# Optimization experiments

Measured on AMD Instinct MI355X. Metric: run time of the kernel, lower is better.

Reference implementation:

```python
import jax, jax.numpy as jnp
import numpy as np

DIM = 384
WIN = 64
HEADS = 12
B_ = 4096


def setup_inputs() -> dict:
    key = jax.random.key(0)
    k1, k2, k3, k4, k5 = jax.random.split(key, 5)
    x = jax.random.normal(k1, (B_, WIN, DIM), dtype=jnp.float32)
    # torch Linear weights: qkv.weight [3*dim, dim], proj.weight [dim, dim], proj.bias [dim]
    qkv_w = jax.random.normal(k2, (3 * DIM, DIM), dtype=jnp.float32) * (DIM ** -0.5)
    proj_w = jax.random.normal(k3, (DIM, DIM), dtype=jnp.float32) * (DIM ** -0.5)
    proj_b = jax.random.normal(k4, (DIM,), dtype=jnp.float32) * 0.02
    bias_table = jax.random.normal(k5, (2 * WIN - 1, HEADS), dtype=jnp.float32) * 0.02
    return {"x": x, "qkv_w": qkv_w, "proj_w": proj_w, "proj_b": proj_b,
            "bias_table": bias_table}


def reference(x, qkv_w, proj_w, proj_b, bias_table):
    B, N, C = x.shape
    H = HEADS
    hd = C // H
    scale = hd ** -0.5
    # qkv projection (torch: x @ W.T), split into q,k,v [B,H,N,hd]
    qkv = jnp.einsum('bnc,dc->bnd', x, qkv_w)
    qkv = qkv.reshape(B, N, 3, H, hd).transpose(2, 0, 3, 1, 4)
    q, k, v = qkv[0] * scale, qkv[1], qkv[2]
    attn = jnp.einsum('bhnd,bhmd->bhnm', q, k)  # [B,H,N,N]
    # relative position bias: index [N,N] into table [2W-1,H]
    coords = jnp.arange(N)
    rel_idx = coords[:, None] - coords[None, :] + (N - 1)  # [N,N]
    bias = bias_table[rel_idx]  # [N,N,H]
    attn = attn + bias.transpose(2, 0, 1)[None]
    attn = jax.nn.softmax(attn, axis=-1)
    out = jnp.einsum('bhnm,bhmd->bhnd', attn, v)
    out = out.transpose(0, 2, 1, 3).reshape(B, N, C)
    out = jnp.einsum('bnc,dc->bnd', out, proj_w) + proj_b
    return out
```

## Files before the change

### kernel.cpp

```cpp
#include <hip/hip_runtime.h>
#include <stdint.h>

#define DIM 384
#define WIN 64
#define HEADS 12
#define HD 32
#define NWIN 4096

typedef _Float16 f16;
typedef unsigned int u32;
typedef _Float16 half8 __attribute__((ext_vector_type(8)));
typedef _Float16 half4 __attribute__((ext_vector_type(4)));
typedef float floatx4 __attribute__((ext_vector_type(4)));

#define AS1 __attribute__((address_space(1)))
#define AS3 __attribute__((address_space(3)))

__device__ __forceinline__ void gl_lds16(const void* g, void* l) {
    __builtin_amdgcn_global_load_lds((const AS1 u32*)g, (AS3 u32*)l, 16, 0, 0);
}

__global__ void cvt_kernel(const float* __restrict__ in, f16* __restrict__ out, long n4) {
    long i = (long)blockIdx.x * blockDim.x + threadIdx.x;
    const long stride = (long)gridDim.x * blockDim.x;
    for (; i < n4; i += stride) {
        float4 v = ((const float4*)in)[i];
        half4 h;
        h[0] = (f16)v.x; h[1] = (f16)v.y; h[2] = (f16)v.z; h[3] = (f16)v.w;
        ((half4*)out)[i] = h;
    }
}

__global__ void pack_w_kernel(const float* __restrict__ w, f16* __restrict__ Bp) {
    const int t = blockIdx.x * 256 + threadIdx.x;
    const int colb = t / 9216;
    const int r1 = t % 9216;
    const int s = r1 / 768;
    const int r2 = r1 % 768;
    const int kc = r2 / 192, u = r2 % 192;
    const float* sp = w + (size_t)(colb * 192 + u) * DIM + s * 32 + kc * 8;
    float4 a = *(const float4*)sp;
    float4 b = *(const float4*)(sp + 4);
    half8 o;
    o[0] = (f16)a.x; o[1] = (f16)a.y; o[2] = (f16)a.z; o[3] = (f16)a.w;
    o[4] = (f16)b.x; o[5] = (f16)b.y; o[6] = (f16)b.z; o[7] = (f16)b.w;
    *(half8*)(Bp + (size_t)t * 8) = o;
}

__global__ void pack_x_kernel(const float* __restrict__ x, f16* __restrict__ Xp) {
    const int b = blockIdx.x;
    const int s = b % 12;
    const int rowb = b / 12;
    const int t = threadIdx.x;
    const int kc = t & 3, rr = t >> 2;
#pragma unroll
    for (int h = 0; h < 2; ++h) {
        const int row = rr + h * 64;
        const float* sp = x + (size_t)(rowb * 128 + row) * DIM + s * 32 + kc * 8;
        float4 a = *(const float4*)sp;
        float4 bq = *(const float4*)(sp + 4);
        half8 o;
        o[0] = (f16)a.x;  o[1] = (f16)a.y;  o[2] = (f16)a.z;  o[3] = (f16)a.w;
        o[4] = (f16)bq.x; o[5] = (f16)bq.y; o[6] = (f16)bq.z; o[7] = (f16)bq.w;
        *(half8*)(Xp + ((size_t)b * 512 + kc * 128 + row) * 8) = o;
    }
}

__global__ void __launch_bounds__(256, 2)
qkv_kernel(const f16* __restrict__ Xp, const f16* __restrict__ Bp,
           f16* __restrict__ q_arr, f16* __restrict__ k_arr,
           f16* __restrict__ v_int, int nwg)
{
    __shared__ __align__(16) f16 ldsA[2][4096];
    __shared__ __align__(16) f16 ldsB[3][6144];

    int lin = blockIdx.x;
    int nlin = lin;
    if ((nwg & 7) == 0) nlin = (lin & 7) * (nwg >> 3) + (lin >> 3);
    const int colb = nlin % 6, rowb = nlin / 6;

    const int tid = threadIdx.x;
    const int wave = tid >> 6, lane = tid & 63;
    const int g = lane >> 4, c = lane & 15;
    const int wm = wave >> 1, wn = wave & 1;

    floatx4 acc[4][6] = {};

    auto stageA = [&](int t) {
        const f16* sa = Xp + (size_t)(rowb * 12 + t) * 4096;
        f16* da = &ldsA[t & 1][0];
#pragma unroll
        for (int r = 0; r < 2; ++r) {
            const int ch = r * 256 + tid;
            gl_lds16(sa + (size_t)ch * 8, da + (size_t)ch * 8);
        }
    };
    auto stageB = [&](int t) {
        const f16* sb = Bp + (size_t)(colb * 12 + t) * 6144;
        f16* db = &ldsB[t % 3][0];
#pragma unroll
        for (int r = 0; r < 3; ++r) {
            const int ch = r * 256 + tid;
            gl_lds16(sb + (size_t)ch * 8, db + (size_t)ch * 8);
        }
    };

    stageA(0); stageB(0); stageB(1);

#pragma unroll
    for (int s = 0; s < 12; ++s) {
        if (s < 11) asm volatile("s_waitcnt vmcnt(3)" ::: "memory");
        else        asm volatile("s_waitcnt vmcnt(0)" ::: "memory");
        __builtin_amdgcn_sched_barrier(0);
        __builtin_amdgcn_s_barrier();
        __builtin_amdgcn_sched_barrier(0);
        if (s < 11) stageA(s + 1);
        if (s < 10) stageB(s + 2);

        half8 af[4], bf[6];
#pragma unroll
        for (int i = 0; i < 4; ++i)
            af[i] = *(const half8*)&ldsA[s & 1][g * 1024 + (wm * 64 + i * 16 + c) * 8];
#pragma unroll
        for (int n = 0; n < 6; ++n)
            bf[n] = *(const half8*)&ldsB[s % 3][g * 1536 + (wn * 96 + n * 16 + c) * 8];
#pragma unroll
        for (int mi = 0; mi < 4; ++mi)
#pragma unroll
            for (int ni = 0; ni < 6; ++ni)
                acc[mi][ni] = __builtin_amdgcn_mfma_f32_16x16x32_f16(
                    af[mi], bf[ni], acc[mi][ni], 0, 0, 0);
    }

    const int which = colb >> 1;
    const int dbase = (colb & 1) * 192;
    const int b0 = rowb * 2 + wm;
    if (which < 2) {
        f16* dst = which ? k_arr : q_arr;
        const float sc = which ? 1.0f : 0.17677669529663687f;
#pragma unroll
        for (int ni = 0; ni < 6; ++ni) {
            const int d = dbase + wn * 96 + ni * 16 + c;
            const int h = d >> 5, e = d & 31;
            f16* base = dst + (size_t)(b0 * HEADS + h) * (WIN * HD) + e;
#pragma unroll
            for (int mi = 0; mi < 4; ++mi)
#pragma unroll
                for (int j = 0; j < 4; ++j) {
                    const int n = mi * 16 + g * 4 + j;
                    base[(size_t)n * HD] = (f16)(acc[mi][ni][j] * sc);
                }
        }
    } else {
#pragma unroll
        for (int ni = 0; ni < 6; ++ni) {
            const int d = dbase + wn * 96 + ni * 16 + c;
            const int h = d >> 5, e = d & 31;
            f16* vb = v_int + (size_t)(b0 * HEADS + h) * (WIN * HD);
#pragma unroll
            for (int mi = 0; mi < 4; ++mi) {
                const int n0 = mi * 16 + g * 4;
                half4 pk;
#pragma unroll
                for (int j = 0; j < 4; ++j) pk[j] = (f16)acc[mi][ni][j];
                *(half4*)(vb + (n0 >> 3) * 256 + e * 8 + (n0 & 7)) = pk;
            }
        }
    }
}

__global__ void proj_kernel(const f16* __restrict__ A, const f16* __restrict__ Bw,
                            float* __restrict__ outp, const float* __restrict__ proj_b,
                            int nwg)
{
    __shared__ __align__(16) f16 lds[3][2][4][128][8];

    int lin = blockIdx.x;
    int nlin = lin;
    if ((nwg & 7) == 0) nlin = (lin & 7) * (nwg >> 3) + (lin >> 3);
    const int colb = nlin % 3, rowb = nlin / 3;
    const int col0 = colb * 128, row0 = rowb * 128;

    const int tid = threadIdx.x;
    const int wave = tid >> 6, lane = tid & 63;
    const int g = lane >> 4, c = lane & 15;
    const int wm = wave >> 1, wn = wave & 1;

    floatx4 acc[4][4] = {};

    auto stage = [&](int t) {
        const int k0 = t * 32;
#pragma unroll
        for (int r = 0; r < 4; ++r) {
            const int u = wave + r * 4;
            const int isB = u >> 3;
            const int uu = u & 7;
            const int kc = uu >> 1, m0 = (uu & 1) * 64;
            const f16* src = (isB ? Bw + (size_t)(col0 + m0 + lane) * DIM
                                  : A  + (size_t)(row0 + m0 + lane) * DIM)
                             + k0 + kc * 8;
            gl_lds16(src, &lds[t % 3][isB][kc][m0][0]);
        }
    };

    stage(0); stage(1);

#pragma unroll
    for (int s = 0; s < 12; ++s) {
        if (s < 11) asm volatile("s_waitcnt vmcnt(4)" ::: "memory");
        else        asm volatile("s_waitcnt vmcnt(0)" ::: "memory");
        asm volatile("s_waitcnt lgkmcnt(0)" ::: "memory");
        __builtin_amdgcn_sched_barrier(0);
        __builtin_amdgcn_s_barrier();
        __builtin_amdgcn_sched_barrier(0);
        if (s < 10) stage(s + 2);

        half8 af[4], bf[4];
#pragma unroll
        for (int i = 0; i < 4; ++i) {
            af[i] = *(const half8*)&lds[s % 3][0][g][wm * 64 + i * 16 + c][0];
            bf[i] = *(const half8*)&lds[s % 3][1][g][wn * 64 + i * 16 + c][0];
        }
#pragma unroll
        for (int mi = 0; mi < 4; ++mi)
#pragma unroll
            for (int ni = 0; ni < 4; ++ni)
                acc[mi][ni] = __builtin_amdgcn_mfma_f32_16x16x32_f16(
                    af[mi], bf[ni], acc[mi][ni], 0, 0, 0);
    }

#pragma unroll
    for (int ni = 0; ni < 4; ++ni) {
        const int d = col0 + wn * 64 + ni * 16 + c;
        const float pb = proj_b[d];
#pragma unroll
        for (int mi = 0; mi < 4; ++mi)
#pragma unroll
            for (int j = 0; j < 4; ++j) {
                const size_t trow = (size_t)row0 + wm * 64 + mi * 16 + g * 4 + j;
                outp[trow * DIM + d] = acc[mi][ni][j] + pb;
            }
    }
}

__global__ void attn_kernel(const f16* __restrict__ q_arr, const f16* __restrict__ k_arr,
                            const f16* __restrict__ v_int,
                            const float* __restrict__ bias_table,
                            f16* __restrict__ attn_out)
{
    const int bid = blockIdx.x;
    const int bw = bid / HEADS, h = bid % HEADS;
    const f16* q = q_arr + (size_t)bid * (WIN * HD);
    const f16* k = k_arr + (size_t)bid * (WIN * HD);
    const f16* v = v_int + (size_t)bid * (WIN * HD);

    const int tid = threadIdx.x;
    const int w = tid >> 6, lane = tid & 63;
    const int g = lane >> 4, c = lane & 15;

    __shared__ float bias_lds[2 * WIN - 1];
    __shared__ __align__(16) f16 p_lds[8][64][8];

    for (int i = tid; i < 2 * WIN - 1; i += 256)
        bias_lds[i] = bias_table[(size_t)i * HEADS + h];
    __syncthreads();

    half8 qa = *(const half8*)(q + (16 * w + c) * HD + g * 8);
    floatx4 s[4];
#pragma unroll
    for (int t = 0; t < 4; ++t) {
        half8 kb = *(const half8*)(k + (16 * t + c) * HD + g * 8);
        floatx4 z = {};
        s[t] = __builtin_amdgcn_mfma_f32_16x16x32_f16(qa, kb, z, 0, 0, 0);
    }

    float pr[4][4];
#pragma unroll
    for (int j = 0; j < 4; ++j) {
        const int n = 16 * w + g * 4 + j;
        float mx = -1e30f;
#pragma unroll
        for (int t = 0; t < 4; ++t) {
            const int m = 16 * t + c;
            pr[j][t] = s[t][j] + bias_lds[n - m + 63];
            mx = fmaxf(mx, pr[j][t]);
        }
        mx = fmaxf(mx, __shfl_xor(mx, 1));
        mx = fmaxf(mx, __shfl_xor(mx, 2));
        mx = fmaxf(mx, __shfl_xor(mx, 4));
        mx = fmaxf(mx, __shfl_xor(mx, 8));
        float sum = 0.f;
#pragma unroll
        for (int t = 0; t < 4; ++t) { pr[j][t] = __expf(pr[j][t] - mx); sum += pr[j][t]; }
        sum += __shfl_xor(sum, 1);
        sum += __shfl_xor(sum, 2);
        sum += __shfl_xor(sum, 4);
        sum += __shfl_xor(sum, 8);
        const float r = 1.0f / sum;
#pragma unroll
        for (int t = 0; t < 4; ++t) {
            const int m = 16 * t + c;
            p_lds[m >> 3][n][m & 7] = (f16)(pr[j][t] * r);
        }
    }
    __syncthreads();

    half8 pa0 = *(const half8*)&p_lds[g][16 * w + c][0];
    half8 pa1 = *(const half8*)&p_lds[4 + g][16 * w + c][0];
    floatx4 o[2];
#pragma unroll
    for (int t = 0; t < 2; ++t) {
        half8 vb0 = *(const half8*)(v + g * 256 + (16 * t + c) * 8);
        half8 vb1 = *(const half8*)(v + (4 + g) * 256 + (16 * t + c) * 8);
        floatx4 z = {};
        o[t] = __builtin_amdgcn_mfma_f32_16x16x32_f16(pa0, vb0, z, 0, 0, 0);
        o[t] = __builtin_amdgcn_mfma_f32_16x16x32_f16(pa1, vb1, o[t], 0, 0, 0);
    }
#pragma unroll
    for (int t = 0; t < 2; ++t)
#pragma unroll
        for (int j = 0; j < 4; ++j) {
            const int n = 16 * w + g * 4 + j;
            attn_out[((size_t)bw * WIN + n) * DIM + h * HD + 16 * t + c] = (f16)o[t][j];
        }
}

extern "C" void kernel_launch(void* const* d_in, const int* in_sizes, int n_in,
                              void* d_out, int out_size, void* d_ws, size_t ws_size,
                              hipStream_t stream) {
    const float* x          = (const float*)d_in[0];
    const float* qkv_w      = (const float*)d_in[1];
    const float* proj_w     = (const float*)d_in[2];
    const float* proj_b     = (const float*)d_in[3];
    const float* bias_table = (const float*)d_in[4];
    float* out = (float*)d_out;
    (void)in_sizes; (void)n_in; (void)out_size;

    uintptr_t p = (uintptr_t)d_ws;
    auto carve = [&](size_t bytes) -> void* {
        uintptr_t q = p; p += (bytes + 255) & ~(size_t)255; return (void*)q;
    };
    f16* w16_proj = (f16*)carve((size_t)DIM * DIM * 2);
    f16* Bp       = (f16*)carve((size_t)6 * 12 * 768 * 8 * 2);
    const size_t fixed = p - (uintptr_t)d_ws;

    int CB = NWIN;
    while (CB > 16 && fixed + (size_t)CB * 245760 + 4096 > ws_size) CB >>= 1;

    f16* Xp = (f16*)carve((size_t)CB * WIN * DIM * 2);
    f16* qa = (f16*)carve((size_t)CB * HEADS * WIN * HD * 2);
    f16* ka = (f16*)carve((size_t)CB * HEADS * WIN * HD * 2);
    f16* vi = (f16*)carve((size_t)CB * HEADS * WIN * HD * 2);
    f16* ao = (f16*)carve((size_t)CB * WIN * DIM * 2);

    cvt_kernel<<<dim3(64), dim3(256), 0, stream>>>(proj_w, w16_proj, (long)(DIM * DIM / 4));
    pack_w_kernel<<<dim3(216), dim3(256), 0, stream>>>(qkv_w, Bp);

    for (int c0 = 0; c0 < NWIN; c0 += CB) {
        const float* xc = x + (size_t)c0 * WIN * DIM;
        const int rowbs = CB / 2;

        pack_x_kernel<<<dim3(rowbs * 12), dim3(256), 0, stream>>>(xc, Xp);

        const int nwg1 = rowbs * 6;
        qkv_kernel<<<dim3(nwg1), dim3(256), 0, stream>>>(Xp, Bp, qa, ka, vi, nwg1);

        attn_kernel<<<dim3(CB * HEADS), dim3(256), 0, stream>>>(qa, ka, vi, bias_table, ao);

        const int nwg2 = rowbs * 3;
        proj_kernel<<<dim3(nwg2), dim3(256), 0, stream>>>(ao, w16_proj,
                                                          out + (size_t)c0 * WIN * DIM, proj_b, nwg2);
    }
}
```

Measured before the change: 957.3 us.

## Enlarge QKV GEMM tile to 256 rows with 512-thread blocks and K=64 stages

The QKV projection kernel now uses 512 threads per block covering 256 rows (four windows) instead of 128. Each pipeline stage loads two K-slabs, so the loop runs 6 iterations of K=64 instead of 12 of K=32. The goal is more reuse of each weight tile per block and fewer barrier and wait points. In exchange, LDS use per block grows to roughly 136 KB, which likely limits occupancy to one block per CU despite the launch bounds asking for two.

```diff
diff --git a/kernel.cpp b/kernel.cpp
--- a/kernel.cpp
+++ b/kernel.cpp
@@ -66,13 +66,13 @@
     }
 }
 
-__global__ void __launch_bounds__(256, 2)
+__global__ void __launch_bounds__(512, 2)
 qkv_kernel(const f16* __restrict__ Xp, const f16* __restrict__ Bp,
            f16* __restrict__ q_arr, f16* __restrict__ k_arr,
            f16* __restrict__ v_int, int nwg)
 {
-    __shared__ __align__(16) f16 ldsA[2][4096];
-    __shared__ __align__(16) f16 ldsB[3][6144];
+    __shared__ __align__(16) f16 ldsA[2][16384];
+    __shared__ __align__(16) f16 ldsB[3][12288];
 
     int lin = blockIdx.x;
     int nlin = lin;
@@ -87,54 +87,66 @@
     floatx4 acc[4][6] = {};
 
     auto stageA = [&](int t) {
-        const f16* sa = Xp + (size_t)(rowb * 12 + t) * 4096;
         f16* da = &ldsA[t & 1][0];
 #pragma unroll
-        for (int r = 0; r < 2; ++r) {
-            const int ch = r * 256 + tid;
-            gl_lds16(sa + (size_t)ch * 8, da + (size_t)ch * 8);
+        for (int r = 0; r < 4; ++r) {
+            const int rg = r >> 1, ss = r & 1;
+            const f16* src = Xp + ((size_t)(2 * rowb + rg) * 12 + (2 * t + ss)) * 4096
+                             + (size_t)tid * 8;
+            gl_lds16(src, da + r * 4096 + tid * 8);
         }
     };
     auto stageB = [&](int t) {
-        const f16* sb = Bp + (size_t)(colb * 12 + t) * 6144;
         f16* db = &ldsB[t % 3][0];
 #pragma unroll
         for (int r = 0; r < 3; ++r) {
-            const int ch = r * 256 + tid;
-            gl_lds16(sb + (size_t)ch * 8, db + (size_t)ch * 8);
+            const int ch = r * 512 + tid;
+            const int ss = ch / 768, rem = ch % 768;
+            const f16* src = Bp + ((size_t)colb * 12 + (2 * t + ss)) * 6144 + (size_t)rem * 8;
+            gl_lds16(src, db + ch * 8);
         }
     };
 
     stageA(0); stageB(0); stageB(1);
 
 #pragma unroll
-    for (int s = 0; s < 12; ++s) {
-        if (s < 11) asm volatile("s_waitcnt vmcnt(3)" ::: "memory");
-        else        asm volatile("s_waitcnt vmcnt(0)" ::: "memory");
+    for (int t = 0; t < 6; ++t) {
+        if (t < 5) asm volatile("s_waitcnt vmcnt(3)" ::: "memory");
+        else       asm volatile("s_waitcnt vmcnt(0)" ::: "memory");
         __builtin_amdgcn_sched_barrier(0);
         __builtin_amdgcn_s_barrier();
         __builtin_amdgcn_sched_barrier(0);
-        if (s < 11) stageA(s + 1);
-        if (s < 10) stageB(s + 2);
-
-        half8 af[4], bf[6];
-#pragma unroll
-        for (int i = 0; i < 4; ++i)
-            af[i] = *(const half8*)&ldsA[s & 1][g * 1024 + (wm * 64 + i * 16 + c) * 8];
-#pragma unroll
-        for (int n = 0; n < 6; ++n)
-            bf[n] = *(const half8*)&ldsB[s % 3][g * 1536 + (wn * 96 + n * 16 + c) * 8];
-#pragma unroll
-        for (int mi = 0; mi < 4; ++mi)
-#pragma unroll
-            for (int ni = 0; ni < 6; ++ni)
-                acc[mi][ni] = __builtin_amdgcn_mfma_f32_16x16x32_f16(
-                    af[mi], bf[ni], acc[mi][ni], 0, 0, 0);
+        if (t < 5) stageA(t + 1);
+        if (t < 4) stageB(t + 2);
+
+        const f16* ab = &ldsA[t & 1][0];
+        const f16* bb = &ldsB[t % 3][0];
+#pragma unroll
+        for (int ks = 0; ks < 2; ++ks) {
+            half8 af[4], bf[6];
+#pragma unroll
+            for (int mi = 0; mi < 4; ++mi) {
+                const int row = wm * 64 + mi * 16 + c;
+                const int slab = (row >> 7) * 2 + ks;
+                af[mi] = *(const half8*)(ab + slab * 4096 + g * 1024 + (row & 127) * 8);
+            }
+#pragma unroll
+            for (int ni = 0; ni < 6; ++ni) {
+                const int u = wn * 96 + ni * 16 + c;
+                bf[ni] = *(const half8*)(bb + ks * 6144 + g * 1536 + u * 8);
+            }
+#pragma unroll
+            for (int mi = 0; mi < 4; ++mi)
+#pragma unroll
+                for (int ni = 0; ni < 6; ++ni)
+                    acc[mi][ni] = __builtin_amdgcn_mfma_f32_16x16x32_f16(
+                        af[mi], bf[ni], acc[mi][ni], 0, 0, 0);
+        }
     }
 
     const int which = colb >> 1;
     const int dbase = (colb & 1) * 192;
-    const int b0 = rowb * 2 + wm;
+    const int b0 = rowb * 4 + wm;
     if (which < 2) {
         f16* dst = which ? k_arr : q_arr;
         const float sc = which ? 1.0f : 0.17677669529663687f;
@@ -362,8 +374,8 @@
 
         pack_x_kernel<<<dim3(rowbs * 12), dim3(256), 0, stream>>>(xc, Xp);
 
-        const int nwg1 = rowbs * 6;
-        qkv_kernel<<<dim3(nwg1), dim3(256), 0, stream>>>(Xp, Bp, qa, ka, vi, nwg1);
+        const int nwg1 = (CB * WIN / 256) * 6;
+        qkv_kernel<<<dim3(nwg1), dim3(512), 0, stream>>>(Xp, Bp, qa, ka, vi, nwg1);
 
         attn_kernel<<<dim3(CB * HEADS), dim3(256), 0, stream>>>(qa, ka, vi, bias_table, ao);
 
```

Result: faster. 915.7 us (-4.3%).
